# Kernel tuning notes

Hardware: AMD Instinct MI355X
Metric: run time of the kernel (lower is better)

## Reference

```python
import jax, jax.numpy as jnp
import numpy as np
import math

B, N, Q, K = 1, 64, 512, 512
C_Q = C_K = C_V = 256
C_HIDDEN = 32
NO_HEADS = 8
HID = C_HIDDEN * NO_HEADS  # 256


def setup_inputs() -> dict:
    key = jax.random.key(0)
    ks = jax.random.split(key, 12)
    inp = {
        "q_x": jax.random.normal(ks[0], (B, N, Q, C_Q), jnp.float32),
        "k_x": jax.random.normal(ks[1], (B, N, K, C_K), jnp.float32),
        "v_x": jax.random.normal(ks[2], (B, N, K, C_V), jnp.float32),
        "bias_mask": jax.random.normal(ks[3], (B, N, 1, 1, K), jnp.float32),
        "bias_pair": jax.random.normal(ks[4], (B, 1, NO_HEADS, Q, K), jnp.float32),
        # projection weights stored [in, out] (torch Linear is [out, in])
        "wq": jax.random.normal(ks[5], (C_Q, HID), jnp.float32) / math.sqrt(C_Q),
        "wk": jax.random.normal(ks[6], (C_K, HID), jnp.float32) / math.sqrt(C_K),
        "wv": jax.random.normal(ks[7], (C_V, HID), jnp.float32) / math.sqrt(C_V),
        # gating: init weights=0, bias=1 in the module; use small random for a non-trivial test
        "wg": jax.random.normal(ks[8], (C_Q, HID), jnp.float32) * 0.02,
        "bg": jnp.ones((HID,), jnp.float32),
        # output: init 'final' (zeros); use small random for a non-trivial test
        "wo": jax.random.normal(ks[9], (HID, C_Q), jnp.float32) * 0.02,
        "bo": jnp.zeros((C_Q,), jnp.float32),
    }
    return inp


def reference(q_x, k_x, v_x, bias_mask, bias_pair, wq, wk, wv, wg, bg, wo, bo):
    h, c = NO_HEADS, C_HIDDEN
    # projections -> [B, N, Q/K, H, C_h]
    q = (q_x @ wq).reshape(*q_x.shape[:-1], h, c) / math.sqrt(c)
    k = (k_x @ wk).reshape(*k_x.shape[:-1], h, c)
    v = (v_x @ wv).reshape(*v_x.shape[:-1], h, c)
    # logits [B, N, H, Q, K] with additive biases
    a = jnp.einsum("bnqhc,bnkhc->bnhqk", q, k) + bias_mask + bias_pair
    a = jax.nn.softmax(a, axis=-1)
    # output [B, N, Q, H, C_h]
    o = jnp.einsum("bnhqk,bnkhc->bnqhc", a, v)
    # gating
    g = jax.nn.sigmoid((q_x @ wg + bg).reshape(*q_x.shape[:-1], h, c))
    o = o * g
    o = o.reshape(*o.shape[:-2], h * c)
    return o @ wo + bo
```

## Files before the change

### kernel.cpp

```cpp
#include <hip/hip_runtime.h>
#include <math.h>

#define NSEQ   64
#define QLEN   512
#define KLEN   512
#define CIN    256
#define HEADS  8
#define CH     32
#define HIDDIM 256
#define M_TOTAL (NSEQ * QLEN)

typedef _Float16 f16x8 __attribute__((ext_vector_type(8)));
typedef _Float16 f16x4 __attribute__((ext_vector_type(4)));
typedef __fp16   fp16x2 __attribute__((ext_vector_type(2)));
typedef float    f32x4 __attribute__((ext_vector_type(4)));

__global__ __launch_bounds__(256) void wcast_kernel(
    const float* __restrict__ w0, const float* __restrict__ w1,
    const float* __restrict__ w2, const float* __restrict__ w3,
    const float* __restrict__ w4, _Float16* __restrict__ wt)
{
    __shared__ float t[64][65];
    const float* W;
    switch (blockIdx.z) {
        case 0: W = w0; break; case 1: W = w1; break;
        case 2: W = w2; break; case 3: W = w3; break;
        default: W = w4;
    }
    _Float16* WT = wt + (size_t)blockIdx.z * 65536;
    const int i0 = blockIdx.x * 64, o0 = blockIdx.y * 64;
    const int tid = threadIdx.x;
    const int rr = tid >> 4, c4 = tid & 15;
    #pragma unroll
    for (int i = 0; i < 4; ++i) {
        const int row = rr + i * 16;
        *(float4*)&t[row][c4 * 4] = *(const float4*)&W[(size_t)(i0 + row) * 256 + o0 + c4 * 4];
    }
    __syncthreads();
    #pragma unroll
    for (int i = 0; i < 4; ++i) {
        const int row = rr + i * 16;
        f16x4 v;
        #pragma unroll
        for (int j = 0; j < 4; ++j) v[j] = (_Float16)t[c4 * 4 + j][row];
        *(f16x4*)&WT[(size_t)(o0 + row) * 256 + i0 + c4 * 4] = v;
    }
}

__global__ __launch_bounds__(256) void bpfrag_kernel(
    const float* __restrict__ bias_pair, float* __restrict__ frag)
{
    __shared__ float t[64][68];
    const int qb = blockIdx.x, kb = blockIdx.y, h = blockIdx.z;
    const int tid = threadIdx.x;
    #pragma unroll
    for (int i = 0; i < 4; ++i) {
        const int idx = tid + i * 256;
        const int r = idx >> 4, c4 = idx & 15;
        *(float4*)&t[r][c4 * 4] = *(const float4*)
            &bias_pair[((size_t)h * QLEN + qb * 64 + r) * KLEN + kb * 64 + c4 * 4];
    }
    __syncthreads();
    const int lane = tid & 63, w = tid >> 6;
    const int l15 = lane & 15, quad = lane >> 4;
    const int qt = qb * 4 + w;
    #pragma unroll
    for (int kt2 = 0; kt2 < 4; ++kt2) {
        const int kt = kb * 4 + kt2;
        float4 v;
        v.x = t[w * 16 + l15][kt2 * 16 + quad * 4 + 0];
        v.y = t[w * 16 + l15][kt2 * 16 + quad * 4 + 1];
        v.z = t[w * 16 + l15][kt2 * 16 + quad * 4 + 2];
        v.w = t[w * 16 + l15][kt2 * 16 + quad * 4 + 3];
        *(float4*)&frag[(((size_t)(h * 32 + qt) * 32) + kt) * 256 + lane * 4] = v;
    }
}

__global__ __launch_bounds__(256, 4) void proj_gemm_kernel(
    const float* __restrict__ q_x, const float* __restrict__ k_x,
    const float* __restrict__ v_x, const _Float16* __restrict__ wT,
    const float* __restrict__ bg,
    _Float16* __restrict__ oq, _Float16* __restrict__ ok,
    _Float16* __restrict__ ov, _Float16* __restrict__ og)
{
    __shared__ _Float16 A_s[128][72];
    __shared__ _Float16 B_s[128][72];
    const int z = blockIdx.z;
    const float* A = (z == 1) ? k_x : (z == 2) ? v_x : q_x;
    const _Float16* BT = wT + (size_t)z * 65536;
    _Float16* C = (z == 0) ? oq : (z == 1) ? ok : (z == 2) ? ov : og;
    const float scale = (z == 0) ? 0.17677669529663689f : 1.0f;

    const int m0 = blockIdx.x * 128, n0 = blockIdx.y * 128;
    const int tid = threadIdx.x;
    const int lane = tid & 63, w = tid >> 6;
    const int l15 = lane & 15, quad = lane >> 4;
    const int mw = (w & 1) * 64, nw = (w >> 1) * 64;

    f32x4 acc[4][4];
    #pragma unroll
    for (int mt = 0; mt < 4; ++mt)
        #pragma unroll
        for (int nt = 0; nt < 4; ++nt) acc[mt][nt] = (f32x4){0.f, 0.f, 0.f, 0.f};

    for (int k0 = 0; k0 < CIN; k0 += 64) {
        __syncthreads();
        #pragma unroll
        for (int it = 0; it < 4; ++it) {
            const int idx = tid + it * 256;
            const int r = idx >> 3, seg = idx & 7;
            const float* ap = A + (size_t)(m0 + r) * CIN + k0 + seg * 8;
            const float4 f0 = *(const float4*)ap;
            const float4 f1 = *(const float4*)(ap + 4);
            f16x8 v;
            v[0] = (_Float16)f0.x; v[1] = (_Float16)f0.y;
            v[2] = (_Float16)f0.z; v[3] = (_Float16)f0.w;
            v[4] = (_Float16)f1.x; v[5] = (_Float16)f1.y;
            v[6] = (_Float16)f1.z; v[7] = (_Float16)f1.w;
            *(f16x8*)&A_s[r][seg * 8] = v;
            *(uint4*)&B_s[r][seg * 8] =
                *(const uint4*)(BT + (size_t)(n0 + r) * CIN + k0 + seg * 8);
        }
        __syncthreads();
        #pragma unroll
        for (int ks = 0; ks < 2; ++ks) {
            f16x8 af[4], bf[4];
            #pragma unroll
            for (int mt = 0; mt < 4; ++mt)
                af[mt] = *(const f16x8*)&A_s[mw + mt * 16 + l15][ks * 32 + quad * 8];
            #pragma unroll
            for (int nt = 0; nt < 4; ++nt)
                bf[nt] = *(const f16x8*)&B_s[nw + nt * 16 + l15][ks * 32 + quad * 8];
            #pragma unroll
            for (int mt = 0; mt < 4; ++mt)
                #pragma unroll
                for (int nt = 0; nt < 4; ++nt)
                    acc[mt][nt] = __builtin_amdgcn_mfma_f32_16x16x32_f16(
                        af[mt], bf[nt], acc[mt][nt], 0, 0, 0);
        }
    }

    #pragma unroll
    for (int mt = 0; mt < 4; ++mt) {
        #pragma unroll
        for (int nt = 0; nt < 4; ++nt) {
            const int col = n0 + nw + nt * 16 + l15;
            const int rowb = m0 + mw + mt * 16 + quad * 4;
            #pragma unroll
            for (int reg = 0; reg < 4; ++reg) {
                float x = acc[mt][nt][reg] * scale;
                if (z == 3) {
                    x += bg[col];
                    x = 1.0f / (1.0f + __expf(-x));
                }
                C[(size_t)(rowb + reg) * HIDDIM + col] = (_Float16)x;
            }
        }
    }
}

__global__ __launch_bounds__(256, 4) void gemm_mfma_kernel(
    const _Float16* __restrict__ Ain, const _Float16* __restrict__ BT,
    const float* __restrict__ bias, float* __restrict__ Cout)
{
    __shared__ _Float16 A_s[128][72];
    __shared__ _Float16 B_s[128][72];
    const int m0 = blockIdx.x * 128, n0 = blockIdx.y * 128;
    const int tid = threadIdx.x;
    const int lane = tid & 63, w = tid >> 6;
    const int l15 = lane & 15, quad = lane >> 4;
    const int mw = (w & 1) * 64, nw = (w >> 1) * 64;

    f32x4 acc[4][4];
    #pragma unroll
    for (int mt = 0; mt < 4; ++mt)
        #pragma unroll
        for (int nt = 0; nt < 4; ++nt) acc[mt][nt] = (f32x4){0.f, 0.f, 0.f, 0.f};

    for (int k0 = 0; k0 < CIN; k0 += 64) {
        __syncthreads();
        #pragma unroll
        for (int it = 0; it < 4; ++it) {
            const int idx = tid + it * 256;
            const int r = idx >> 3, seg = idx & 7;
            *(uint4*)&A_s[r][seg * 8] =
                *(const uint4*)(Ain + (size_t)(m0 + r) * CIN + k0 + seg * 8);
            *(uint4*)&B_s[r][seg * 8] =
                *(const uint4*)(BT + (size_t)(n0 + r) * CIN + k0 + seg * 8);
        }
        __syncthreads();
        #pragma unroll
        for (int ks = 0; ks < 2; ++ks) {
            f16x8 af[4], bf[4];
            #pragma unroll
            for (int mt = 0; mt < 4; ++mt)
                af[mt] = *(const f16x8*)&A_s[mw + mt * 16 + l15][ks * 32 + quad * 8];
            #pragma unroll
            for (int nt = 0; nt < 4; ++nt)
                bf[nt] = *(const f16x8*)&B_s[nw + nt * 16 + l15][ks * 32 + quad * 8];
            #pragma unroll
            for (int mt = 0; mt < 4; ++mt)
                #pragma unroll
                for (int nt = 0; nt < 4; ++nt)
                    acc[mt][nt] = __builtin_amdgcn_mfma_f32_16x16x32_f16(
                        af[mt], bf[nt], acc[mt][nt], 0, 0, 0);
        }
    }

    #pragma unroll
    for (int mt = 0; mt < 4; ++mt) {
        #pragma unroll
        for (int nt = 0; nt < 4; ++nt) {
            const int col = n0 + nw + nt * 16 + l15;
            const int rowb = m0 + mw + mt * 16 + quad * 4;
            #pragma unroll
            for (int reg = 0; reg < 4; ++reg) {
                const float x = acc[mt][nt][reg] + bias[col];
                Cout[(size_t)(rowb + reg) * HIDDIM + col] = x;
            }
        }
    }
}

__global__ __launch_bounds__(256) void vtrans_kernel(
    const _Float16* __restrict__ v, _Float16* __restrict__ vT)
{
    __shared__ _Float16 t[32][72];
    const int nh = blockIdx.x;
    const int n = nh >> 3, h = nh & 7;
    const int tid = threadIdx.x;
    for (int kc = 0; kc < KLEN; kc += 64) {
        __syncthreads();
        const int r = tid >> 2, c8 = (tid & 3) * 8;
        const f16x8 vv = *(const f16x8*)(v + (size_t)(n * KLEN + kc + r) * HIDDIM + h * CH + c8);
        #pragma unroll
        for (int j = 0; j < 8; ++j) t[c8 + j][r] = vv[j];
        __syncthreads();
        const int c = tid >> 3, k8 = (tid & 7) * 8;
        const f16x8 o = *(const f16x8*)&t[c][k8];
        *(f16x8*)(vT + ((size_t)nh * CH + c) * KLEN + kc + k8) = o;
    }
}

__global__ __launch_bounds__(256, 4) void attn_kernel(
    const _Float16* __restrict__ qb, const _Float16* __restrict__ kb,
    const _Float16* __restrict__ vT, const _Float16* __restrict__ gb,
    _Float16* __restrict__ ob,
    const float* __restrict__ bias_mask, const float* __restrict__ bp_frag)
{
    __shared__ _Float16 k_s[128][40];
    __shared__ _Float16 v_s[32][136];

    const int n    = blockIdx.x;
    const int h    = blockIdx.y;
    const int q0   = blockIdx.z * 128;
    const int tid  = threadIdx.x;
    const int lane = tid & 63;
    const int wq   = tid >> 6;
    const int l15  = lane & 15;
    const int quad = lane >> 4;

    f16x8 qf[2];
    #pragma unroll
    for (int qt = 0; qt < 2; ++qt)
        qf[qt] = *(const f16x8*)(qb +
            (size_t)(n * QLEN + q0 + wq * 32 + qt * 16 + l15) * HIDDIM + h * CH + quad * 8);

    const float* bpf = bp_frag +
        ((size_t)(h * 32 + blockIdx.z * 8 + wq * 2) * 32) * 256 + lane * 4;
    const float* bmb = bias_mask + n * KLEN + quad * 4;

    f32x4 o_acc[2][2];
    float l_lane[2] = {0.f, 0.f};
    #pragma unroll
    for (int qt = 0; qt < 2; ++qt)
        #pragma unroll
        for (int ct = 0; ct < 2; ++ct) o_acc[qt][ct] = (f32x4){0.f, 0.f, 0.f, 0.f};

    const f32x4 z4 = (f32x4){0.f, 0.f, 0.f, 0.f};

    for (int ch = 0; ch < 4; ++ch) {
        __syncthreads();
        #pragma unroll
        for (int i = 0; i < 2; ++i) {
            const int idx = tid + i * 256;
            const int r = idx >> 2, c8 = idx & 3;
            *(uint4*)&k_s[r][c8 * 8] = *(const uint4*)
                (kb + (size_t)(n * KLEN + ch * 128 + r) * HIDDIM + h * CH + c8 * 8);
            const int vr = idx >> 4, vs = idx & 15;
            *(uint4*)&v_s[vr][vs * 8] = *(const uint4*)
                (vT + ((size_t)(n * HEADS + h) * CH + vr) * KLEN + ch * 128 + vs * 8);
        }
        __syncthreads();

        #pragma unroll
        for (int kt = 0; kt < 8; ++kt) {
            const int kti = ch * 8 + kt;
            const f16x8 kf = *(const f16x8*)&k_s[kt * 16 + l15][quad * 8];
            const f32x4 s0 = __builtin_amdgcn_mfma_f32_16x16x32_f16(kf, qf[0], z4, 0, 0, 0);
            const f32x4 s1 = __builtin_amdgcn_mfma_f32_16x16x32_f16(kf, qf[1], z4, 0, 0, 0);
            const float4 bm = *(const float4*)(bmb + ch * 128 + kt * 16);
            const f16x4 bv0 = *(const f16x4*)&v_s[l15][kt * 16 + quad * 4];
            const f16x4 bv1 = *(const f16x4*)&v_s[16 + l15][kt * 16 + quad * 4];
            #pragma unroll
            for (int qt = 0; qt < 2; ++qt) {
                const f32x4 s = qt ? s1 : s0;
                const float4 bp = *(const float4*)(bpf + ((size_t)qt * 32 + kti) * 256);
                const float p0 = __expf(s[0] + bm.x + bp.x - 4.0f);
                const float p1 = __expf(s[1] + bm.y + bp.y - 4.0f);
                const float p2 = __expf(s[2] + bm.z + bp.z - 4.0f);
                const float p3 = __expf(s[3] + bm.w + bp.w - 4.0f);
                l_lane[qt] += (p0 + p1) + (p2 + p3);
                union { f16x4 v; fp16x2 h[2]; } u;
                u.h[0] = __builtin_amdgcn_cvt_pkrtz(p0, p1);
                u.h[1] = __builtin_amdgcn_cvt_pkrtz(p2, p3);
                o_acc[qt][0] = __builtin_amdgcn_mfma_f32_16x16x16f16(u.v, bv0, o_acc[qt][0], 0, 0, 0);
                o_acc[qt][1] = __builtin_amdgcn_mfma_f32_16x16x16f16(u.v, bv1, o_acc[qt][1], 0, 0, 0);
            }
        }
    }

    float invl[2][4];
    #pragma unroll
    for (int qt = 0; qt < 2; ++qt) {
        float lf = l_lane[qt];
        lf += __shfl_xor(lf, 16);
        lf += __shfl_xor(lf, 32);
        #pragma unroll
        for (int reg = 0; reg < 4; ++reg)
            invl[qt][reg] = 1.0f / __shfl(lf, quad * 4 + reg);
    }

    #pragma unroll
    for (int qt = 0; qt < 2; ++qt) {
        #pragma unroll
        for (int ct = 0; ct < 2; ++ct) {
            #pragma unroll
            for (int reg = 0; reg < 4; ++reg) {
                const int row = q0 + wq * 32 + qt * 16 + quad * 4 + reg;
                const size_t idx = (size_t)(n * QLEN + row) * HIDDIM + h * CH + ct * 16 + l15;
                const float g = (float)gb[idx];
                ob[idx] = (_Float16)(o_acc[qt][ct][reg] * invl[qt][reg] * g);
            }
        }
    }
}

extern "C" void kernel_launch(void* const* d_in, const int* in_sizes, int n_in,
                              void* d_out, int out_size, void* d_ws, size_t ws_size,
                              hipStream_t stream)
{
    const float* q_x       = (const float*)d_in[0];
    const float* k_x       = (const float*)d_in[1];
    const float* v_x       = (const float*)d_in[2];
    const float* bias_mask = (const float*)d_in[3];
    const float* bias_pair = (const float*)d_in[4];
    const float* wq        = (const float*)d_in[5];
    const float* wk        = (const float*)d_in[6];
    const float* wv        = (const float*)d_in[7];
    const float* wg        = (const float*)d_in[8];
    const float* bg        = (const float*)d_in[9];
    const float* wo        = (const float*)d_in[10];
    const float* bo        = (const float*)d_in[11];
    float* out = (float*)d_out;

    const size_t BUF = (size_t)M_TOTAL * HIDDIM;
    _Float16* ws_q  = (_Float16*)d_ws;
    _Float16* ws_k  = ws_q + BUF;
    _Float16* ws_v  = ws_k + BUF;
    _Float16* ws_vT = ws_v + BUF;
    _Float16* ws_g  = ws_vT + BUF;
    _Float16* ws_o  = ws_g + BUF;
    _Float16* wT    = ws_o + BUF;
    float*    bpf   = (float*)(wT + 5 * 65536);

    wcast_kernel<<<dim3(4, 4, 5), 256, 0, stream>>>(wq, wk, wv, wg, wo, wT);
    bpfrag_kernel<<<dim3(8, 8, 8), 256, 0, stream>>>(bias_pair, bpf);

    proj_gemm_kernel<<<dim3(M_TOTAL / 128, 2, 4), 256, 0, stream>>>(
        q_x, k_x, v_x, wT, bg, ws_q, ws_k, ws_v, ws_g);

    vtrans_kernel<<<dim3(NSEQ * HEADS), 256, 0, stream>>>(ws_v, ws_vT);

    attn_kernel<<<dim3(NSEQ, HEADS, QLEN / 128), 256, 0, stream>>>(
        ws_q, ws_k, ws_vT, ws_g, ws_o, bias_mask, bpf);

    gemm_mfma_kernel<<<dim3(M_TOTAL / 128, 2), 256, 0, stream>>>(
        ws_o, wT + 4 * 65536, bo, out);
}
```

Measured before the change: 287.6 us.

## Double-buffer GEMMs with direct global-to-LDS loads and fuse V transpose

Both projection and output GEMMs now stage tiles through double-buffered LDS, using direct global-to-LDS loads with an XOR swizzle for fp16 tiles and register prefetch for the fp32 activation tiles, so the next K-slice loads overlap MFMA work. The projection kernel writes V directly in transposed layout, removing the separate transpose kernel and its extra round-trip through memory. Weight ordering and grid mapping are rearranged so q and g share q_x blocks. Larger LDS footprints lower the occupancy hint from 4 to 2 blocks per CU, and the transposed V stores are 8-byte scattered writes.

```diff
diff --git a/kernel.cpp b/kernel.cpp
--- a/kernel.cpp
+++ b/kernel.cpp
@@ -15,6 +15,12 @@
 typedef __fp16   fp16x2 __attribute__((ext_vector_type(2)));
 typedef float    f32x4 __attribute__((ext_vector_type(4)));
 
+__device__ __forceinline__ void gload16(const void* g, void* l) {
+    __builtin_amdgcn_global_load_lds(
+        (const __attribute__((address_space(1))) void*)g,
+        (__attribute__((address_space(3))) void*)l, 16, 0, 0);
+}
+
 __global__ __launch_bounds__(256) void wcast_kernel(
     const float* __restrict__ w0, const float* __restrict__ w1,
     const float* __restrict__ w2, const float* __restrict__ w3,
@@ -76,21 +82,143 @@
     }
 }
 
-__global__ __launch_bounds__(256, 4) void proj_gemm_kernel(
+__global__ __launch_bounds__(256, 2) void proj_gemm_kernel(
     const float* __restrict__ q_x, const float* __restrict__ k_x,
     const float* __restrict__ v_x, const _Float16* __restrict__ wT,
     const float* __restrict__ bg,
     _Float16* __restrict__ oq, _Float16* __restrict__ ok,
-    _Float16* __restrict__ ov, _Float16* __restrict__ og)
+    _Float16* __restrict__ ovT, _Float16* __restrict__ og)
 {
     __shared__ _Float16 A_s[128][72];
-    __shared__ _Float16 B_s[128][72];
-    const int z = blockIdx.z;
-    const float* A = (z == 1) ? k_x : (z == 2) ? v_x : q_x;
-    const _Float16* BT = wT + (size_t)z * 65536;
-    _Float16* C = (z == 0) ? oq : (z == 1) ? ok : (z == 2) ? ov : og;
-    const float scale = (z == 0) ? 0.17677669529663689f : 1.0f;
-
+    __shared__ __attribute__((aligned(16))) _Float16 B_s[2][128 * 64];
+
+    const int mode = (blockIdx.z << 1) | (blockIdx.y >> 1);
+    const float* A = (mode <= 1) ? q_x : (mode == 2) ? k_x : v_x;
+    const _Float16* BT = wT + (size_t)mode * 65536;
+    const int m0 = blockIdx.x * 128;
+    const int n0 = (blockIdx.y & 1) * 128;
+    const int tid = threadIdx.x;
+    const int lane = tid & 63, w = tid >> 6;
+    const int l15 = lane & 15, quad = lane >> 4;
+    const int mw = (w & 1) * 64, nw = (w >> 1) * 64;
+    const int ar = tid >> 3, aseg = tid & 7;
+
+    f32x4 acc[4][4];
+    #pragma unroll
+    for (int mt = 0; mt < 4; ++mt)
+        #pragma unroll
+        for (int nt = 0; nt < 4; ++nt) acc[mt][nt] = (f32x4){0.f, 0.f, 0.f, 0.f};
+
+    float4 alo[4], ahi[4];
+    #pragma unroll
+    for (int it = 0; it < 4; ++it) {
+        const float* ap = A + (size_t)(m0 + ar + it * 32) * CIN + aseg * 8;
+        alo[it] = *(const float4*)ap;
+        ahi[it] = *(const float4*)(ap + 4);
+    }
+    #pragma unroll
+    for (int j = 0; j < 4; ++j) {
+        const int p = tid + j * 256;
+        const int r = p >> 3;
+        const int lc = (p & 7) ^ (r & 7);
+        gload16(BT + (size_t)(n0 + r) * CIN + lc * 8, &B_s[0][p * 8]);
+    }
+    #pragma unroll
+    for (int it = 0; it < 4; ++it) {
+        f16x8 v;
+        v[0] = (_Float16)alo[it].x; v[1] = (_Float16)alo[it].y;
+        v[2] = (_Float16)alo[it].z; v[3] = (_Float16)alo[it].w;
+        v[4] = (_Float16)ahi[it].x; v[5] = (_Float16)ahi[it].y;
+        v[6] = (_Float16)ahi[it].z; v[7] = (_Float16)ahi[it].w;
+        *(f16x8*)&A_s[ar + it * 32][aseg * 8] = v;
+    }
+    __syncthreads();
+
+    int buf = 0;
+    for (int kk = 0; kk < 4; ++kk) {
+        if (kk < 3) {
+            const int k0n = (kk + 1) * 64;
+            #pragma unroll
+            for (int it = 0; it < 4; ++it) {
+                const float* ap = A + (size_t)(m0 + ar + it * 32) * CIN + k0n + aseg * 8;
+                alo[it] = *(const float4*)ap;
+                ahi[it] = *(const float4*)(ap + 4);
+            }
+            #pragma unroll
+            for (int j = 0; j < 4; ++j) {
+                const int p = tid + j * 256;
+                const int r = p >> 3;
+                const int lc = (p & 7) ^ (r & 7);
+                gload16(BT + (size_t)(n0 + r) * CIN + k0n + lc * 8, &B_s[buf ^ 1][p * 8]);
+            }
+        }
+        #pragma unroll
+        for (int ks = 0; ks < 2; ++ks) {
+            f16x8 af[4], bf[4];
+            #pragma unroll
+            for (int mt = 0; mt < 4; ++mt)
+                af[mt] = *(const f16x8*)&A_s[mw + mt * 16 + l15][ks * 32 + quad * 8];
+            #pragma unroll
+            for (int nt = 0; nt < 4; ++nt) {
+                const int brow = nw + nt * 16 + l15;
+                const int bc = (ks * 4 + quad) ^ (brow & 7);
+                bf[nt] = *(const f16x8*)&B_s[buf][brow * 64 + bc * 8];
+            }
+            #pragma unroll
+            for (int mt = 0; mt < 4; ++mt)
+                #pragma unroll
+                for (int nt = 0; nt < 4; ++nt)
+                    acc[mt][nt] = __builtin_amdgcn_mfma_f32_16x16x32_f16(
+                        af[mt], bf[nt], acc[mt][nt], 0, 0, 0);
+        }
+        if (kk < 3) {
+            __syncthreads();
+            #pragma unroll
+            for (int it = 0; it < 4; ++it) {
+                f16x8 v;
+                v[0] = (_Float16)alo[it].x; v[1] = (_Float16)alo[it].y;
+                v[2] = (_Float16)alo[it].z; v[3] = (_Float16)alo[it].w;
+                v[4] = (_Float16)ahi[it].x; v[5] = (_Float16)ahi[it].y;
+                v[6] = (_Float16)ahi[it].z; v[7] = (_Float16)ahi[it].w;
+                *(f16x8*)&A_s[ar + it * 32][aseg * 8] = v;
+            }
+            __syncthreads();
+            buf ^= 1;
+        }
+    }
+
+    #pragma unroll
+    for (int mt = 0; mt < 4; ++mt) {
+        #pragma unroll
+        for (int nt = 0; nt < 4; ++nt) {
+            const int col = n0 + nw + nt * 16 + l15;
+            const int rowb = m0 + mw + mt * 16 + quad * 4;
+            if (mode == 3) {
+                const int nn = rowb >> 9, kpos = rowb & 511;
+                f16x4 st;
+                #pragma unroll
+                for (int reg = 0; reg < 4; ++reg) st[reg] = (_Float16)acc[mt][nt][reg];
+                *(f16x4*)&ovT[((size_t)(nn * 256 + col)) * 512 + kpos] = st;
+            } else {
+                _Float16* C = (mode == 0) ? oq : (mode == 1) ? og : ok;
+                #pragma unroll
+                for (int reg = 0; reg < 4; ++reg) {
+                    float x = acc[mt][nt][reg];
+                    if (mode == 0) x *= 0.17677669529663689f;
+                    if (mode == 1) { x += bg[col]; x = 1.0f / (1.0f + __expf(-x)); }
+                    C[(size_t)(rowb + reg) * HIDDIM + col] = (_Float16)x;
+                }
+            }
+        }
+    }
+}
+
+__global__ __launch_bounds__(256, 2) void gemm_mfma_kernel(
+    const _Float16* __restrict__ Ain, const _Float16* __restrict__ BT,
+    const float* __restrict__ bias, float* __restrict__ Cout)
+{
+    __shared__ __attribute__((aligned(16))) _Float16 A_s[2][128 * 64];
+    __shared__ __attribute__((aligned(16))) _Float16 B_s[2][128 * 64];
     const int m0 = blockIdx.x * 128, n0 = blockIdx.y * 128;
     const int tid = threadIdx.x;
     const int lane = tid & 63, w = tid >> 6;
@@ -103,34 +231,44 @@
         #pragma unroll
         for (int nt = 0; nt < 4; ++nt) acc[mt][nt] = (f32x4){0.f, 0.f, 0.f, 0.f};
 
-    for (int k0 = 0; k0 < CIN; k0 += 64) {
-        __syncthreads();
-        #pragma unroll
-        for (int it = 0; it < 4; ++it) {
-            const int idx = tid + it * 256;
-            const int r = idx >> 3, seg = idx & 7;
-            const float* ap = A + (size_t)(m0 + r) * CIN + k0 + seg * 8;
-            const float4 f0 = *(const float4*)ap;
-            const float4 f1 = *(const float4*)(ap + 4);
-            f16x8 v;
-            v[0] = (_Float16)f0.x; v[1] = (_Float16)f0.y;
-            v[2] = (_Float16)f0.z; v[3] = (_Float16)f0.w;
-            v[4] = (_Float16)f1.x; v[5] = (_Float16)f1.y;
-            v[6] = (_Float16)f1.z; v[7] = (_Float16)f1.w;
-            *(f16x8*)&A_s[r][seg * 8] = v;
-            *(uint4*)&B_s[r][seg * 8] =
-                *(const uint4*)(BT + (size_t)(n0 + r) * CIN + k0 + seg * 8);
-        }
-        __syncthreads();
+    #pragma unroll
+    for (int j = 0; j < 4; ++j) {
+        const int p = tid + j * 256;
+        const int r = p >> 3;
+        const int lc = (p & 7) ^ (r & 7);
+        gload16(Ain + (size_t)(m0 + r) * CIN + lc * 8, &A_s[0][p * 8]);
+        gload16(BT  + (size_t)(n0 + r) * CIN + lc * 8, &B_s[0][p * 8]);
+    }
+    __syncthreads();
+
+    int buf = 0;
+    for (int kk = 0; kk < 4; ++kk) {
+        if (kk < 3) {
+            const int k0n = (kk + 1) * 64;
+            #pragma unroll
+            for (int j = 0; j < 4; ++j) {
+                const int p = tid + j * 256;
+                const int r = p >> 3;
+                const int lc = (p & 7) ^ (r & 7);
+                gload16(Ain + (size_t)(m0 + r) * CIN + k0n + lc * 8, &A_s[buf ^ 1][p * 8]);
+                gload16(BT  + (size_t)(n0 + r) * CIN + k0n + lc * 8, &B_s[buf ^ 1][p * 8]);
+            }
+        }
         #pragma unroll
         for (int ks = 0; ks < 2; ++ks) {
             f16x8 af[4], bf[4];
             #pragma unroll
-            for (int mt = 0; mt < 4; ++mt)
-                af[mt] = *(const f16x8*)&A_s[mw + mt * 16 + l15][ks * 32 + quad * 8];
-            #pragma unroll
-            for (int nt = 0; nt < 4; ++nt)
-                bf[nt] = *(const f16x8*)&B_s[nw + nt * 16 + l15][ks * 32 + quad * 8];
+            for (int mt = 0; mt < 4; ++mt) {
+                const int arow = mw + mt * 16 + l15;
+                const int ac = (ks * 4 + quad) ^ (arow & 7);
+                af[mt] = *(const f16x8*)&A_s[buf][arow * 64 + ac * 8];
+            }
+            #pragma unroll
+            for (int nt = 0; nt < 4; ++nt) {
+                const int brow = nw + nt * 16 + l15;
+                const int bc = (ks * 4 + quad) ^ (brow & 7);
+                bf[nt] = *(const f16x8*)&B_s[buf][brow * 64 + bc * 8];
+            }
             #pragma unroll
             for (int mt = 0; mt < 4; ++mt)
                 #pragma unroll
@@ -138,6 +276,7 @@
                     acc[mt][nt] = __builtin_amdgcn_mfma_f32_16x16x32_f16(
                         af[mt], bf[nt], acc[mt][nt], 0, 0, 0);
         }
+        if (kk < 3) { __syncthreads(); buf ^= 1; }
     }
 
     #pragma unroll
@@ -148,97 +287,10 @@
             const int rowb = m0 + mw + mt * 16 + quad * 4;
             #pragma unroll
             for (int reg = 0; reg < 4; ++reg) {
-                float x = acc[mt][nt][reg] * scale;
-                if (z == 3) {
-                    x += bg[col];
-                    x = 1.0f / (1.0f + __expf(-x));
-                }
-                C[(size_t)(rowb + reg) * HIDDIM + col] = (_Float16)x;
-            }
-        }
-    }
-}
-
-__global__ __launch_bounds__(256, 4) void gemm_mfma_kernel(
-    const _Float16* __restrict__ Ain, const _Float16* __restrict__ BT,
-    const float* __restrict__ bias, float* __restrict__ Cout)
-{
-    __shared__ _Float16 A_s[128][72];
-    __shared__ _Float16 B_s[128][72];
-    const int m0 = blockIdx.x * 128, n0 = blockIdx.y * 128;
-    const int tid = threadIdx.x;
-    const int lane = tid & 63, w = tid >> 6;
-    const int l15 = lane & 15, quad = lane >> 4;
-    const int mw = (w & 1) * 64, nw = (w >> 1) * 64;
-
-    f32x4 acc[4][4];
-    #pragma unroll
-    for (int mt = 0; mt < 4; ++mt)
-        #pragma unroll
-        for (int nt = 0; nt < 4; ++nt) acc[mt][nt] = (f32x4){0.f, 0.f, 0.f, 0.f};
-
-    for (int k0 = 0; k0 < CIN; k0 += 64) {
-        __syncthreads();
-        #pragma unroll
-        for (int it = 0; it < 4; ++it) {
-            const int idx = tid + it * 256;
-            const int r = idx >> 3, seg = idx & 7;
-            *(uint4*)&A_s[r][seg * 8] =
-                *(const uint4*)(Ain + (size_t)(m0 + r) * CIN + k0 + seg * 8);
-            *(uint4*)&B_s[r][seg * 8] =
-                *(const uint4*)(BT + (size_t)(n0 + r) * CIN + k0 + seg * 8);
-        }
-        __syncthreads();
-        #pragma unroll
-        for (int ks = 0; ks < 2; ++ks) {
-            f16x8 af[4], bf[4];
-            #pragma unroll
-            for (int mt = 0; mt < 4; ++mt)
-                af[mt] = *(const f16x8*)&A_s[mw + mt * 16 + l15][ks * 32 + quad * 8];
-            #pragma unroll
-            for (int nt = 0; nt < 4; ++nt)
-                bf[nt] = *(const f16x8*)&B_s[nw + nt * 16 + l15][ks * 32 + quad * 8];
-            #pragma unroll
-            for (int mt = 0; mt < 4; ++mt)
-                #pragma unroll
-                for (int nt = 0; nt < 4; ++nt)
-                    acc[mt][nt] = __builtin_amdgcn_mfma_f32_16x16x32_f16(
-                        af[mt], bf[nt], acc[mt][nt], 0, 0, 0);
-        }
-    }
-
-    #pragma unroll
-    for (int mt = 0; mt < 4; ++mt) {
-        #pragma unroll
-        for (int nt = 0; nt < 4; ++nt) {
-            const int col = n0 + nw + nt * 16 + l15;
-            const int rowb = m0 + mw + mt * 16 + quad * 4;
-            #pragma unroll
-            for (int reg = 0; reg < 4; ++reg) {
                 const float x = acc[mt][nt][reg] + bias[col];
                 Cout[(size_t)(rowb + reg) * HIDDIM + col] = x;
             }
         }
-    }
-}
-
-__global__ __launch_bounds__(256) void vtrans_kernel(
-    const _Float16* __restrict__ v, _Float16* __restrict__ vT)
-{
-    __shared__ _Float16 t[32][72];
-    const int nh = blockIdx.x;
-    const int n = nh >> 3, h = nh & 7;
-    const int tid = threadIdx.x;
-    for (int kc = 0; kc < KLEN; kc += 64) {
-        __syncthreads();
-        const int r = tid >> 2, c8 = (tid & 3) * 8;
-        const f16x8 vv = *(const f16x8*)(v + (size_t)(n * KLEN + kc + r) * HIDDIM + h * CH + c8);
-        #pragma unroll
-        for (int j = 0; j < 8; ++j) t[c8 + j][r] = vv[j];
-        __syncthreads();
-        const int c = tid >> 3, k8 = (tid & 7) * 8;
-        const f16x8 o = *(const f16x8*)&t[c][k8];
-        *(f16x8*)(vT + ((size_t)nh * CH + c) * KLEN + kc + k8) = o;
     }
 }
 
@@ -367,20 +419,17 @@
     const size_t BUF = (size_t)M_TOTAL * HIDDIM;
     _Float16* ws_q  = (_Float16*)d_ws;
     _Float16* ws_k  = ws_q + BUF;
-    _Float16* ws_v  = ws_k + BUF;
-    _Float16* ws_vT = ws_v + BUF;
+    _Float16* ws_vT = ws_k + BUF;
     _Float16* ws_g  = ws_vT + BUF;
     _Float16* ws_o  = ws_g + BUF;
     _Float16* wT    = ws_o + BUF;
     float*    bpf   = (float*)(wT + 5 * 65536);
 
-    wcast_kernel<<<dim3(4, 4, 5), 256, 0, stream>>>(wq, wk, wv, wg, wo, wT);
+    wcast_kernel<<<dim3(4, 4, 5), 256, 0, stream>>>(wq, wg, wk, wv, wo, wT);
     bpfrag_kernel<<<dim3(8, 8, 8), 256, 0, stream>>>(bias_pair, bpf);
 
-    proj_gemm_kernel<<<dim3(M_TOTAL / 128, 2, 4), 256, 0, stream>>>(
-        q_x, k_x, v_x, wT, bg, ws_q, ws_k, ws_v, ws_g);
-
-    vtrans_kernel<<<dim3(NSEQ * HEADS), 256, 0, stream>>>(ws_v, ws_vT);
+    proj_gemm_kernel<<<dim3(M_TOTAL / 128, 4, 2), 256, 0, stream>>>(
+        q_x, k_x, v_x, wT, bg, ws_q, ws_k, ws_vT, ws_g);
 
     attn_kernel<<<dim3(NSEQ, HEADS, QLEN / 128), 256, 0, stream>>>(
         ws_q, ws_k, ws_vT, ws_g, ws_o, bias_mask, bpf);
```

Result: faster. 272.5 us (-5.3%).
